# Kernel optimization log

Hardware: AMD Instinct MI355X
Metric: run time of the kernel (lower is better)

Reference implementation:

```python
import jax, jax.numpy as jnp
import numpy as np

B, T, IN, H = 64, 128, 64, 256  # batch, seq_len, input_size, hidden_size
G = 4 * H                        # gate dim


def setup_inputs() -> dict:
    key = jax.random.key(0)
    ks = jax.random.split(key, 8)
    f32 = jnp.float32

    def p(k, shape, scale=0.05):
        return (jax.random.normal(k, shape, dtype=f32) * scale)

    # forget-gate bias initialized to 1.0 (slice [H:2H]) as in the torch module
    b_mu = jnp.zeros((G,), f32).at[H:2 * H].set(1.0)
    lv = lambda shape: jnp.full(shape, -3.0, f32)  # logvar init = -3.0

    return {
        "x": jax.random.normal(ks[0], (B, T, IN), dtype=f32),
        # layer 0
        "w_ih_mu0": p(ks[1], (G, IN)),
        "w_ih_lv0": lv((G, IN)),
        "w_hh_mu0": p(ks[2], (G, H)),
        "w_hh_lv0": lv((G, H)),
        "b_ih_mu0": b_mu,
        "b_ih_lv0": lv((G,)),
        "b_hh_mu0": jnp.zeros((G,), f32),
        "b_hh_lv0": lv((G,)),
        # layer 1 (input size = H since unidirectional)
        "w_ih_mu1": p(ks[3], (G, H)),
        "w_ih_lv1": lv((G, H)),
        "w_hh_mu1": p(ks[4], (G, H)),
        "w_hh_lv1": lv((G, H)),
        "b_ih_mu1": b_mu,
        "b_ih_lv1": lv((G,)),
        "b_hh_mu1": jnp.zeros((G,), f32),
        "b_hh_lv1": lv((G,)),
    }


def _sample(mu, logvar, k):
    # reparameterization: mu + exp(0.5*logvar) * eps, fresh eps every call (every timestep)
    return mu + jnp.exp(0.5 * logvar) * jax.random.normal(k, mu.shape, mu.dtype)


def _lstm_layer(x_seq, wih_mu, wih_lv, whh_mu, whh_lv,
                bih_mu, bih_lv, bhh_mu, bhh_lv, layer_key):
    # x_seq: (T, B, in) -> (hs (T,B,H), h_T (B,H), c_T (B,H))
    Tn, Bn = x_seq.shape[0], x_seq.shape[1]
    Hn = whh_mu.shape[1]
    keys = jax.random.split(layer_key, Tn)
    h0 = jnp.zeros((Bn, Hn), x_seq.dtype)
    c0 = jnp.zeros((Bn, Hn), x_seq.dtype)

    def step(carry, inp):
        h, c = carry
        x_t, k = inp
        k1, k2, k3, k4 = jax.random.split(k, 4)
        wih = _sample(wih_mu, wih_lv, k1)
        whh = _sample(whh_mu, whh_lv, k2)
        bih = _sample(bih_mu, bih_lv, k3)
        bhh = _sample(bhh_mu, bhh_lv, k4)
        gates = x_t @ wih.T + bih + h @ whh.T + bhh  # (B, 4H)
        i, f, g, o = jnp.split(gates, 4, axis=-1)
        c = jax.nn.sigmoid(f) * c + jax.nn.sigmoid(i) * jnp.tanh(g)
        h = jax.nn.sigmoid(o) * jnp.tanh(c)
        return (h, c), h

    (hT, cT), hs = jax.lax.scan(step, (h0, c0), (x_seq, keys))
    return hs, hT, cT


def reference(x,
              w_ih_mu0, w_ih_lv0, w_hh_mu0, w_hh_lv0,
              b_ih_mu0, b_ih_lv0, b_hh_mu0, b_hh_lv0,
              w_ih_mu1, w_ih_lv1, w_hh_mu1, w_hh_lv1,
              b_ih_mu1, b_ih_lv1, b_hh_mu1, b_hh_lv1):
    base = jax.random.key(42)
    x_seq = jnp.transpose(x, (1, 0, 2))  # batch_first -> (T, B, IN)
    hs0, h0T, c0T = _lstm_layer(x_seq, w_ih_mu0, w_ih_lv0, w_hh_mu0, w_hh_lv0,
                                b_ih_mu0, b_ih_lv0, b_hh_mu0, b_hh_lv0,
                                jax.random.fold_in(base, 0))
    hs1, h1T, c1T = _lstm_layer(hs0, w_ih_mu1, w_ih_lv1, w_hh_mu1, w_hh_lv1,
                                b_ih_mu1, b_ih_lv1, b_hh_mu1, b_hh_lv1,
                                jax.random.fold_in(base, 1))
    output = jnp.transpose(hs1, (1, 0, 2))  # (B, T, H)
    h_n = jnp.stack([h0T, h1T])  # (num_layers, B, H)
    c_n = jnp.stack([c0T, c1T])
    return output, h_n, c_n
```

## Files before the change

kernel.cpp:

```cpp
#include <hip/hip_runtime.h>
#include <stdint.h>


typedef unsigned int u32;
typedef unsigned long long u64;
typedef float f32x4 __attribute__((ext_vector_type(4)));

#define Bn 64
#define Tn 128
#define INn 64
#define Hn 256
#define Gn 1024
#define BH (Bn * Hn)

#define OFF_ELV_WIH0 0
#define OFF_ELV_WHH0 65536
#define OFF_ELV_WIH1 327680
#define OFF_ELV_WHH1 589824
#define OFF_ELV_B    851968
#define OFF_H0       856064
#define OFF_H1       (OFF_H0 + 2 * BH)
#define OFF_KEYS     (OFF_H1 + 2 * BH)
#define OFF_SLOTS    (OFF_KEYS + 2 * Tn * 8)
#define OFF_GO       (OFF_SLOTS + 256 * 32)
#define WS_FLOATS    (OFF_GO + 64)
#define STATE_FLOATS (OFF_KEYS - OFF_H0)
#define OUT_HN       (Bn * Tn * Hn)

struct KP { u32 a, b; };

__device__ __forceinline__ void st_coh(float* p, float v) {
  __hip_atomic_store(p, v, __ATOMIC_RELAXED, __HIP_MEMORY_SCOPE_AGENT);
}
__device__ __forceinline__ u32 ld_flag(const u32* p) {
  return __hip_atomic_load(p, __ATOMIC_RELAXED, __HIP_MEMORY_SCOPE_AGENT);
}
__device__ __forceinline__ void st_flag(u32* p, u32 v) {
  __hip_atomic_store(p, v, __ATOMIC_RELAXED, __HIP_MEMORY_SCOPE_AGENT);
}

__device__ __forceinline__ KP tf(u32 k0, u32 k1, u32 x0, u32 x1) {
  u32 ks2 = k0 ^ k1 ^ 0x1BD11BDAu;
  x0 += k0; x1 += k1;
#define TFR(r) { x0 += x1; x1 = (x1 << (r)) | (x1 >> (32 - (r))); x1 ^= x0; }
  TFR(13) TFR(15) TFR(26) TFR(6)
  x0 += k1;  x1 += ks2 + 1u;
  TFR(17) TFR(29) TFR(16) TFR(24)
  x0 += ks2; x1 += k0 + 2u;
  TFR(13) TFR(15) TFR(26) TFR(6)
  x0 += k0;  x1 += k1 + 3u;
  TFR(17) TFR(29) TFR(16) TFR(24)
  x0 += k1;  x1 += ks2 + 4u;
  TFR(13) TFR(15) TFR(26) TFR(6)
  x0 += ks2; x1 += k0 + 5u;
#undef TFR
  KP o; o.a = x0; o.b = x1; return o;
}

__device__ __forceinline__ float n01(u32 bits) {
  float f = __uint_as_float((bits >> 9) | 0x3f800000u) - 1.0f;
  float u = fmaxf(-0.99999994f, f * 2.0f - 0.99999994f);
  float w = -log1pf(-u * u);
  float p;
  if (w < 5.0f) {
    float z = w - 2.5f;
    p = 2.81022636e-08f;
    p = 3.43273939e-07f  + p * z;
    p = -3.5233877e-06f  + p * z;
    p = -4.39150654e-06f + p * z;
    p = 0.00021858087f   + p * z;
    p = -0.00125372503f  + p * z;
    p = -0.00417768164f  + p * z;
    p = 0.246640727f     + p * z;
    p = 1.50140941f      + p * z;
  } else {
    float z = sqrtf(w) - 3.0f;
    p = -0.000200214257f;
    p = 0.000100950558f  + p * z;
    p = 0.00134934322f   + p * z;
    p = -0.00367342844f  + p * z;
    p = 0.00573950773f   + p * z;
    p = -0.0076224613f   + p * z;
    p = 0.00943887047f   + p * z;
    p = 1.00167406f      + p * z;
    p = 2.83297682f      + p * z;
  }
  return 1.41421356237f * (p * u);
}

#define POOL_BYTES 51360
#define WBUF_OFF   0
#define INB_OFF    16512
#define BIAS_OFF   51328

template<int LAYER>
__device__ __forceinline__ void sample_weights(
    const float* __restrict__ wihmu, const float* __restrict__ whhmu,
    const float* __restrict__ bihmu, const float* __restrict__ bhhmu,
    const float* __restrict__ ws, float* __restrict__ wbuf,
    float* __restrict__ bias2, int ts, int j0, int tid)
{
  constexpr int Kin  = LAYER ? Hn : INn;
  constexpr int Ktot = Kin + Hn;
  if (ts >= Tn) return;
  const u32* kp = (const u32*)(ws + OFF_KEYS) + (LAYER * Tn + ts) * 8;
  const float* elv_ih  = ws + (LAYER ? OFF_ELV_WIH1 : OFF_ELV_WIH0);
  const float* elv_hh  = ws + (LAYER ? OFF_ELV_WHH1 : OFF_ELV_WHH0);
  const float* belv_ih = ws + OFF_ELV_B + LAYER * 2048;
  const float* belv_hh = belv_ih + 1024;

  const int k = tid;
  if (k < Ktot) {
    bool iswih = k < Kin;
    u32 ka = iswih ? kp[0] : kp[2], kb = iswih ? kp[1] : kp[3];
    const float* mup  = iswih ? wihmu  : whhmu;
    const float* elvp = iswih ? elv_ih : elv_hh;
    int kk = iswih ? k : k - Kin;
    int kstride = iswih ? Kin : Hn;
    #pragma unroll
    for (int gi = 0; gi < 8; ++gi) {
      int g = (gi & 3) * Hn + j0 + (gi >> 2);
      int i = g * kstride + kk;
      KP r = tf(ka, kb, 0u, (u32)i);
      wbuf[gi * 516 + k] = mup[i] + elvp[i] * n01(r.a ^ r.b);
    }
  }
  if (tid < 8) {
    int g = (tid & 3) * Hn + j0 + (tid >> 2);
    KP rb = tf(kp[4], kp[5], 0u, (u32)g);
    KP rh = tf(kp[6], kp[7], 0u, (u32)g);
    bias2[tid] = bihmu[g] + belv_ih[g] * n01(rb.a ^ rb.b)
               + bhhmu[g] + belv_hh[g] * n01(rh.a ^ rh.b);
  }
}

template<int LAYER>
__device__ void step_body(
    const float* __restrict__ x,
    float* __restrict__ ws, float* __restrict__ out, int t, char* pool,
    float& creg, const u32* go_other)
{
  constexpr int Kin  = LAYER ? Hn : INn;
  constexpr int Ktot = Kin + Hn;
  constexpr int nch  = Ktot / 64;
  const int tid = threadIdx.x;
  const int lb  = blockIdx.x & 127;
  const int j0  = lb * 2;
  const int ts  = LAYER ? (t - 1) : t;

  float* wbuf  = (float*)(pool + WBUF_OFF);
  float* inb   = (float*)(pool + INB_OFF);
  float* gpart = (float*)(pool + INB_OFF);
  float* bias2 = (float*)(pool + BIAS_OFF);

  const float* hprev = ws + (LAYER ? OFF_H1 : OFF_H0) + (ts & 1) * BH;
  const float* h0in  = ws + OFF_H0 + ((ts + 1) & 1) * BH;

  f32x4 pfA[2], pfB[2];
  auto issue = [&](int c, f32x4* pf) {
    #pragma unroll
    for (int m = 0; m < 2; ++m) {
      int f = tid + 512 * m, b = f >> 4, q4 = (f & 15) * 4;
      if (LAYER == 0) {
        if (c == 0) {
          const float* p = x + (b * Tn + ts) * INn + q4;
          asm volatile("global_load_dwordx4 %0, %1, off"
                       : "=v"(pf[m]) : "v"(p) : "memory");
        } else {
          const float* p = hprev + b * Hn + (c - 1) * 64 + q4;
          asm volatile("global_load_dwordx4 %0, %1, off sc1"
                       : "=v"(pf[m]) : "v"(p) : "memory");
        }
      } else {
        const float* p = (c < 4) ? (h0in + b * Hn + c * 64 + q4)
                                 : (hprev + b * Hn + (c - 4) * 64 + q4);
        asm volatile("global_load_dwordx4 %0, %1, off sc1"
                     : "=v"(pf[m]) : "v"(p) : "memory");
      }
    }
  };
  auto writeb = [&](int c, f32x4* pf) {
    #pragma unroll
    for (int m = 0; m < 2; ++m) {
      int f = tid + 512 * m, b = f >> 4, seg = f & 15;
      int col = 4 * (seg ^ ((b >> 3) & 7));
      *(f32x4*)&inb[(((c & 1) << 6) + b) * 68 + col] = pf[m];
    }
  };

  issue(0, pfA);
  if (nch > 1) issue(1, pfB);
  if (nch > 1) asm volatile("s_waitcnt vmcnt(2)" ::: "memory");
  else         asm volatile("s_waitcnt vmcnt(0)" ::: "memory");
  __builtin_amdgcn_sched_barrier(0);
  writeb(0, pfA);
  __syncthreads();

  const int kq    = tid >> 5;
  const int bp    = (tid >> 2) & 7;
  const int rhalf = (tid >> 1) & 1;
  const int jj    = tid & 1;
  const int colq  = 4 * (kq ^ bp);

  float acc[4][4];
  #pragma unroll
  for (int r = 0; r < 4; ++r)
    acc[r][0] = acc[r][1] = acc[r][2] = acc[r][3] = 0.f;

  #pragma unroll
  for (int c = 0; c < nch; ++c) {
    f32x4* cur = (c & 1) ? pfB : pfA;
    f32x4* nxt = (c & 1) ? pfA : pfB;
    if (c + 2 < nch) issue(c + 2, cur);
    float4 w4[4];
    #pragma unroll
    for (int s = 0; s < 4; ++s)
      w4[s] = *(const float4*)&wbuf[(jj * 4 + s) * 516 + c * 64 + kq * 4];
    #pragma unroll
    for (int rr = 0; rr < 4; ++rr) {
      int b = bp * 8 + rhalf * 4 + rr;
      float4 in4 = *(const float4*)&inb[(((c & 1) << 6) + b) * 68 + colq];
      #pragma unroll
      for (int s = 0; s < 4; ++s)
        acc[rr][s] += in4.x * w4[s].x + in4.y * w4[s].y
                    + in4.z * w4[s].z + in4.w * w4[s].w;
    }
    if (c + 1 < nch) {
      if (c + 2 < nch) asm volatile("s_waitcnt vmcnt(2)" ::: "memory");
      else             asm volatile("s_waitcnt vmcnt(0)" ::: "memory");
      __builtin_amdgcn_sched_barrier(0);
      writeb(c + 1, nxt);
    }
    __syncthreads();
  }

  if (LAYER == 0) {
    if (tid == 0) {
      while (ld_flag(go_other) < (u32)t)
        __builtin_amdgcn_s_sleep(1);
    }
    asm volatile("" ::: "memory");
  }

  #pragma unroll
  for (int rr = 0; rr < 4; ++rr) {
    int r = rhalf * 4 + rr;
    float4 v = {acc[rr][0], acc[rr][1], acc[rr][2], acc[rr][3]};
    int col4 = (bp * 16 + r * 2 + jj) ^ bp;
    *(float4*)&gpart[kq * 520 + col4 * 4] = v;
  }
  __syncthreads();

  if (tid < 128) {
    const int b = tid >> 1, j2 = tid & 1;
    const int rbp = b >> 3, rr = b & 7;
    const int col4 = (rbp * 16 + rr * 2 + j2) ^ rbp;
    float4 gq = {0.f, 0.f, 0.f, 0.f};
    #pragma unroll
    for (int q = 0; q < 16; ++q) {
      float4 p = *(const float4*)&gpart[q * 520 + col4 * 4];
      gq.x += p.x; gq.y += p.y; gq.z += p.z; gq.w += p.w;
    }
    const int j = j0 + j2;
    float gI = gq.x + bias2[j2 * 4 + 0];
    float gF = gq.y + bias2[j2 * 4 + 1];
    float gG = gq.z + bias2[j2 * 4 + 2];
    float gO = gq.w + bias2[j2 * 4 + 3];

    float cp = creg;
    float si = 1.f / (1.f + expf(-gI));
    float sf = 1.f / (1.f + expf(-gF));
    float so = 1.f / (1.f + expf(-gO));
    float cn = sf * cp + si * tanhf(gG);
    float hn = so * tanhf(cn);
    creg = cn;
    float* hnx = ws + (LAYER ? OFF_H1 : OFF_H0) + ((ts + 1) & 1) * BH;
    st_coh(hnx + b * Hn + j, hn);
    if (LAYER == 0) {
      if (ts == Tn - 1) {
        out[OUT_HN + b * Hn + j] = hn;
        out[OUT_HN + 2 * BH + b * Hn + j] = cn;
      }
    } else {
      out[b * (Tn * Hn) + ts * Hn + j] = hn;
      if (ts == Tn - 1) {
        out[OUT_HN + BH + b * Hn + j] = hn;
        out[OUT_HN + 3 * BH + b * Hn + j] = cn;
      }
    }
  }
}

__global__ __launch_bounds__(512) void bayes_lstm_persist(
    const float* __restrict__ x,
    const float* __restrict__ wihmu0, const float* __restrict__ whhmu0,
    const float* __restrict__ bihmu0, const float* __restrict__ bhhmu0,
    const float* __restrict__ wihmu1, const float* __restrict__ whhmu1,
    const float* __restrict__ bihmu1, const float* __restrict__ bhhmu1,
    float* __restrict__ ws, float* __restrict__ out)
{
  __shared__ __align__(16) char pool[POOL_BYTES];
  const int tid = threadIdx.x, bid = blockIdx.x;
  const int layer = bid >> 7, j0 = (bid & 127) * 2;
  float* wbuf  = (float*)(pool + WBUF_OFF);
  float* bias2 = (float*)(pool + BIAS_OFF);
  u32* slots = (u32*)(ws + OFF_SLOTS);
  u32* go0   = (u32*)(ws + OFF_GO);
  u32* go1   = (u32*)(ws + OFF_GO) + 32;
  float creg = 0.f;

  if (layer == 0)
    sample_weights<0>(wihmu0, whhmu0, bihmu0, bhhmu0, ws, wbuf, bias2, 0, j0, tid);
  __syncthreads();

  for (int t = 0; t <= Tn; ++t) {
    if (layer == 0) {
      if (t < Tn) step_body<0>(x, ws, out, t, pool, creg, go1);
    } else {
      if (t >= 1) step_body<1>(x, ws, out, t, pool, creg, go0);
    }
    if (t == Tn) break;

    __syncthreads();
    if (tid == 0) st_flag(slots + bid * 32, (u32)(t + 1));

    if (layer == 0)
      sample_weights<0>(wihmu0, whhmu0, bihmu0, bhhmu0, ws, wbuf, bias2,
                        t + 1, j0, tid);
    else
      sample_weights<1>(wihmu1, whhmu1, bihmu1, bhhmu1, ws, wbuf, bias2,
                        t, j0, tid);

    if (bid == 0) {
      if (tid < 128) {
        u32* myslot = slots + tid * 32;
        while (ld_flag(myslot) < (u32)(t + 1))
          __builtin_amdgcn_s_sleep(1);
      }
      asm volatile("" ::: "memory");
      __syncthreads();
      if (tid == 0) st_flag(go0, (u32)(t + 1));
    } else if (bid == 128) {
      if (tid < 128) {
        u32* myslot = slots + (128 + tid) * 32;
        while (ld_flag(myslot) < (u32)(t + 1))
          __builtin_amdgcn_s_sleep(1);
      }
      asm volatile("" ::: "memory");
      __syncthreads();
      if (tid == 0) st_flag(go1, (u32)(t + 1));
      if (tid == 0) {
        while (ld_flag(go0) < (u32)(t + 1))
          __builtin_amdgcn_s_sleep(1);
      }
      asm volatile("" ::: "memory");
    } else if (layer == 0) {
      if (tid == 0) {
        while (ld_flag(go0) < (u32)(t + 1))
          __builtin_amdgcn_s_sleep(1);
      }
      asm volatile("" ::: "memory");
    } else {
      if (tid == 0) {
        while (ld_flag(go1) < (u32)(t + 1))
          __builtin_amdgcn_s_sleep(1);
        while (ld_flag(go0) < (u32)(t + 1))
          __builtin_amdgcn_s_sleep(1);
      }
      asm volatile("" ::: "memory");
    }
    __syncthreads();
  }
}

__global__ __launch_bounds__(256) void bayes_lstm_prologue(
    const float* __restrict__ wihlv0, const float* __restrict__ whhlv0,
    const float* __restrict__ bihlv0, const float* __restrict__ bhhlv0,
    const float* __restrict__ wihlv1, const float* __restrict__ whhlv1,
    const float* __restrict__ bihlv1, const float* __restrict__ bhhlv1,
    float* __restrict__ ws)
{
  const int gt = blockIdx.x * 256 + threadIdx.x;
  const int stride = gridDim.x * 256;
  for (int i = gt; i < 65536; i += stride)
    ws[OFF_ELV_WIH0 + i] = expf(0.5f * wihlv0[i]);
  for (int i = gt; i < 262144; i += stride) {
    ws[OFF_ELV_WHH0 + i] = expf(0.5f * whhlv0[i]);
    ws[OFF_ELV_WIH1 + i] = expf(0.5f * wihlv1[i]);
    ws[OFF_ELV_WHH1 + i] = expf(0.5f * whhlv1[i]);
  }
  for (int i = gt; i < 1024; i += stride) {
    ws[OFF_ELV_B + i]        = expf(0.5f * bihlv0[i]);
    ws[OFF_ELV_B + 1024 + i] = expf(0.5f * bhhlv0[i]);
    ws[OFF_ELV_B + 2048 + i] = expf(0.5f * bihlv1[i]);
    ws[OFF_ELV_B + 3072 + i] = expf(0.5f * bhhlv1[i]);
  }
  for (int i = gt; i < STATE_FLOATS; i += stride)
    st_coh(ws + OFF_H0 + i, 0.f);
  for (int i = gt; i < 256 * 32 + 64; i += stride)
    st_flag((u32*)(ws + OFF_SLOTS) + i, 0u);
  if (gt < 2 * Tn) {
    int l = gt >> 7, ts = gt & 127;
    KP lk  = tf(0u, 42u, 0u, (u32)l);
    KP kt  = tf(lk.a, lk.b, 0u, (u32)ts);
    KP kw  = tf(kt.a, kt.b, 0u, 0u);
    KP ku  = tf(kt.a, kt.b, 0u, 1u);
    KP kbi = tf(kt.a, kt.b, 0u, 2u);
    KP kbh = tf(kt.a, kt.b, 0u, 3u);
    u32* kp = (u32*)(ws + OFF_KEYS) + gt * 8;
    kp[0] = kw.a;  kp[1] = kw.b;  kp[2] = ku.a;  kp[3] = ku.b;
    kp[4] = kbi.a; kp[5] = kbi.b; kp[6] = kbh.a; kp[7] = kbh.b;
  }
}

extern "C" void kernel_launch(void* const* d_in, const int* in_sizes, int n_in,
                              void* d_out, int out_size, void* d_ws, size_t ws_size,
                              hipStream_t stream) {
  (void)in_sizes; (void)n_in; (void)out_size;
  if (ws_size < (size_t)WS_FLOATS * sizeof(float)) return;

  const float* x      = (const float*)d_in[0];
  const float* wihmu0 = (const float*)d_in[1];
  const float* wihlv0 = (const float*)d_in[2];
  const float* whhmu0 = (const float*)d_in[3];
  const float* whhlv0 = (const float*)d_in[4];
  const float* bihmu0 = (const float*)d_in[5];
  const float* bihlv0 = (const float*)d_in[6];
  const float* bhhmu0 = (const float*)d_in[7];
  const float* bhhlv0 = (const float*)d_in[8];
  const float* wihmu1 = (const float*)d_in[9];
  const float* wihlv1 = (const float*)d_in[10];
  const float* whhmu1 = (const float*)d_in[11];
  const float* whhlv1 = (const float*)d_in[12];
  const float* bihmu1 = (const float*)d_in[13];
  const float* bihlv1 = (const float*)d_in[14];
  const float* bhhmu1 = (const float*)d_in[15];
  const float* bhhlv1 = (const float*)d_in[16];
  float* ws  = (float*)d_ws;
  float* out = (float*)d_out;

  bayes_lstm_prologue<<<dim3(256), dim3(256), 0, stream>>>(
      wihlv0, whhlv0, bihlv0, bhhlv0, wihlv1, whhlv1, bihlv1, bhhlv1, ws);

  bayes_lstm_persist<<<dim3(256), dim3(512), 0, stream>>>(
      x, wihmu0, whhmu0, bihmu0, bhhmu0,
      wihmu1, whhmu1, bihmu1, bhhmu1, ws, out);
}
```

Baseline: 2.011 ms.

## Replace two-level go-flag barrier with direct slot polling and deepen prefetch

Drops the aggregator blocks (bid 0 and bid 128) that collected per-block slot flags and published go0/go1. Every block now polls all 128 relevant slot flags directly using 128 threads, which removes one hop of flag latency from each timestep's grid barrier. The cost is many more concurrent atomic loads hitting the same flag lines. The input prefetch pipeline also grows from two buffers to four chunks in flight, with matching vmcnt waits, at the cost of more registers.

```diff
diff --git a/kernel.cpp b/kernel.cpp
--- a/kernel.cpp
+++ b/kernel.cpp
@@ -3,7 +3,6 @@
 
 
 typedef unsigned int u32;
-typedef unsigned long long u64;
 typedef float f32x4 __attribute__((ext_vector_type(4)));
 
 #define Bn 64
@@ -22,8 +21,7 @@
 #define OFF_H1       (OFF_H0 + 2 * BH)
 #define OFF_KEYS     (OFF_H1 + 2 * BH)
 #define OFF_SLOTS    (OFF_KEYS + 2 * Tn * 8)
-#define OFF_GO       (OFF_SLOTS + 256 * 32)
-#define WS_FLOATS    (OFF_GO + 64)
+#define WS_FLOATS    (OFF_SLOTS + 256 * 32)
 #define STATE_FLOATS (OFF_KEYS - OFF_H0)
 #define OUT_HN       (Bn * Tn * Hn)
 
@@ -136,9 +134,9 @@
 
 template<int LAYER>
 __device__ void step_body(
-    const float* __restrict__ x,
-    float* __restrict__ ws, float* __restrict__ out, int t, char* pool,
-    float& creg, const u32* go_other)
+    const float* x,
+    float* ws, float* out, int t, char* pool,
+    float& creg, u32* slots)
 {
   constexpr int Kin  = LAYER ? Hn : INn;
   constexpr int Ktot = Kin + Hn;
@@ -156,7 +154,7 @@
   const float* hprev = ws + (LAYER ? OFF_H1 : OFF_H0) + (ts & 1) * BH;
   const float* h0in  = ws + OFF_H0 + ((ts + 1) & 1) * BH;
 
-  f32x4 pfA[2], pfB[2];
+  f32x4 pf0[2], pf1[2], pf2[2], pf3[2];
   auto issue = [&](int c, f32x4* pf) {
     #pragma unroll
     for (int m = 0; m < 2; ++m) {
@@ -179,6 +177,14 @@
       }
     }
   };
+  auto pfsel = [&](int c) -> f32x4* {
+    switch (c & 3) {
+      case 0: return pf0;
+      case 1: return pf1;
+      case 2: return pf2;
+      default: return pf3;
+    }
+  };
   auto writeb = [&](int c, f32x4* pf) {
     #pragma unroll
     for (int m = 0; m < 2; ++m) {
@@ -188,12 +194,10 @@
     }
   };
 
-  issue(0, pfA);
-  if (nch > 1) issue(1, pfB);
-  if (nch > 1) asm volatile("s_waitcnt vmcnt(2)" ::: "memory");
-  else         asm volatile("s_waitcnt vmcnt(0)" ::: "memory");
+  issue(0, pf0); issue(1, pf1); issue(2, pf2); issue(3, pf3);
+  asm volatile("s_waitcnt vmcnt(6)" ::: "memory");
   __builtin_amdgcn_sched_barrier(0);
-  writeb(0, pfA);
+  writeb(0, pf0);
   __syncthreads();
 
   const int kq    = tid >> 5;
@@ -209,9 +213,7 @@
 
   #pragma unroll
   for (int c = 0; c < nch; ++c) {
-    f32x4* cur = (c & 1) ? pfB : pfA;
-    f32x4* nxt = (c & 1) ? pfA : pfB;
-    if (c + 2 < nch) issue(c + 2, cur);
+    if (c + 4 < nch) issue(c + 4, pfsel(c + 4));
     float4 w4[4];
     #pragma unroll
     for (int s = 0; s < 4; ++s)
@@ -226,17 +228,22 @@
                     + in4.z * w4[s].z + in4.w * w4[s].w;
     }
     if (c + 1 < nch) {
-      if (c + 2 < nch) asm volatile("s_waitcnt vmcnt(2)" ::: "memory");
-      else             asm volatile("s_waitcnt vmcnt(0)" ::: "memory");
+      constexpr int last = nch - 1;
+      const int hi = (c + 4 < last) ? (c + 4) : last;
+      const int rem = hi - (c + 1);
+      if (rem >= 3)      asm volatile("s_waitcnt vmcnt(6)" ::: "memory");
+      else if (rem == 2) asm volatile("s_waitcnt vmcnt(4)" ::: "memory");
+      else if (rem == 1) asm volatile("s_waitcnt vmcnt(2)" ::: "memory");
+      else               asm volatile("s_waitcnt vmcnt(0)" ::: "memory");
       __builtin_amdgcn_sched_barrier(0);
-      writeb(c + 1, nxt);
+      writeb(c + 1, pfsel(c + 1));
     }
     __syncthreads();
   }
 
   if (LAYER == 0) {
-    if (tid == 0) {
-      while (ld_flag(go_other) < (u32)t)
+    if (tid < 128) {
+      while (ld_flag(slots + (128 + tid) * 32) < (u32)t)
         __builtin_amdgcn_s_sleep(1);
     }
     asm volatile("" ::: "memory");
@@ -305,8 +312,6 @@
   float* wbuf  = (float*)(pool + WBUF_OFF);
   float* bias2 = (float*)(pool + BIAS_OFF);
   u32* slots = (u32*)(ws + OFF_SLOTS);
-  u32* go0   = (u32*)(ws + OFF_GO);
-  u32* go1   = (u32*)(ws + OFF_GO) + 32;
   float creg = 0.f;
 
   if (layer == 0)
@@ -315,9 +320,9 @@
 
   for (int t = 0; t <= Tn; ++t) {
     if (layer == 0) {
-      if (t < Tn) step_body<0>(x, ws, out, t, pool, creg, go1);
+      if (t < Tn) step_body<0>(x, ws, out, t, pool, creg, slots);
     } else {
-      if (t >= 1) step_body<1>(x, ws, out, t, pool, creg, go0);
+      if (t >= 1) step_body<1>(x, ws, out, t, pool, creg, slots);
     }
     if (t == Tn) break;
 
@@ -331,44 +336,18 @@
       sample_weights<1>(wihmu1, whhmu1, bihmu1, bhhmu1, ws, wbuf, bias2,
                         t, j0, tid);
 
-    if (bid == 0) {
-      if (tid < 128) {
-        u32* myslot = slots + tid * 32;
-        while (ld_flag(myslot) < (u32)(t + 1))
+    if (tid < 128) {
+      if (layer == 0) {
+        while (ld_flag(slots + tid * 32) < (u32)(t + 1))
+          __builtin_amdgcn_s_sleep(1);
+      } else {
+        while (ld_flag(slots + (128 + tid) * 32) < (u32)(t + 1))
+          __builtin_amdgcn_s_sleep(1);
+        while (ld_flag(slots + tid * 32) < (u32)(t + 1))
           __builtin_amdgcn_s_sleep(1);
       }
-      asm volatile("" ::: "memory");
-      __syncthreads();
-      if (tid == 0) st_flag(go0, (u32)(t + 1));
-    } else if (bid == 128) {
-      if (tid < 128) {
-        u32* myslot = slots + (128 + tid) * 32;
-        while (ld_flag(myslot) < (u32)(t + 1))
-          __builtin_amdgcn_s_sleep(1);
-      }
-      asm volatile("" ::: "memory");
-      __syncthreads();
-      if (tid == 0) st_flag(go1, (u32)(t + 1));
-      if (tid == 0) {
-        while (ld_flag(go0) < (u32)(t + 1))
-          __builtin_amdgcn_s_sleep(1);
-      }
-      asm volatile("" ::: "memory");
-    } else if (layer == 0) {
-      if (tid == 0) {
-        while (ld_flag(go0) < (u32)(t + 1))
-          __builtin_amdgcn_s_sleep(1);
-      }
-      asm volatile("" ::: "memory");
-    } else {
-      if (tid == 0) {
-        while (ld_flag(go1) < (u32)(t + 1))
-          __builtin_amdgcn_s_sleep(1);
-        while (ld_flag(go0) < (u32)(t + 1))
-          __builtin_amdgcn_s_sleep(1);
-      }
-      asm volatile("" ::: "memory");
-    }
+    }
+    asm volatile("" ::: "memory");
     __syncthreads();
   }
 }
@@ -397,7 +376,7 @@
   }
   for (int i = gt; i < STATE_FLOATS; i += stride)
     st_coh(ws + OFF_H0 + i, 0.f);
-  for (int i = gt; i < 256 * 32 + 64; i += stride)
+  for (int i = gt; i < 256 * 32; i += stride)
     st_flag((u32*)(ws + OFF_SLOTS) + i, 0u);
   if (gt < 2 * Tn) {
     int l = gt >> 7, ts = gt & 127;
```

After: 2.073 ms. 1.03x slower.
